# Kernel optimization log

Measured on AMD Instinct MI355X. Metric: run time of the kernel, lower is better.

The kernel has to match this reference:

```python
import jax, jax.numpy as jnp
import numpy as np

D_MODEL = 1024
N_HEADS = 16
D_K = D_MODEL // N_HEADS
B, S = 2, 2048
NEG = -1.0e9


def setup_inputs() -> dict:
    key = jax.random.key(0)
    ks = jax.random.split(key, 12)
    sc = 1.0 / np.sqrt(D_MODEL)
    inp = {
        'query': jax.random.normal(ks[0], (B, S, D_MODEL), jnp.float32),
        'key': jax.random.normal(ks[1], (B, S, D_MODEL), jnp.float32),
        'value': jax.random.normal(ks[2], (B, S, D_MODEL), jnp.float32),
        # causal mask, broadcast over batch: 1 = attend, 0 = masked
        'mask': jnp.broadcast_to(jnp.tril(jnp.ones((S, S), jnp.int32)), (B, S, S)),
        'wq': jax.random.normal(ks[3], (D_MODEL, D_MODEL), jnp.float32) * sc,
        'bq': jnp.zeros((D_MODEL,), jnp.float32),
        'wk': jax.random.normal(ks[4], (D_MODEL, D_MODEL), jnp.float32) * sc,
        'bk': jnp.zeros((D_MODEL,), jnp.float32),
        'wv': jax.random.normal(ks[5], (D_MODEL, D_MODEL), jnp.float32) * sc,
        'bv': jnp.zeros((D_MODEL,), jnp.float32),
        'wo': jax.random.normal(ks[6], (D_MODEL, D_MODEL), jnp.float32) * sc,
        'bo': jnp.zeros((D_MODEL,), jnp.float32),
    }
    return inp


def reference(query, key, value, mask, wq, bq, wk, bk, wv, bv, wo, bo):
    b, sq, _ = query.shape
    sk = key.shape[1]
    # linear projections, split into heads: [B, H, S, d_k]
    def proj(x, w, bias, s):
        return (x @ w + bias).reshape(b, s, N_HEADS, D_K).transpose(0, 2, 1, 3)
    Q = proj(query, wq, bq, sq)
    K = proj(key, wk, bk, sk)
    V = proj(value, wv, bv, sk)
    # scaled dot-product attention with full score matrix [B, H, Sq, Sk]
    scores = jnp.einsum('bhqd,bhkd->bhqk', Q, K) / np.sqrt(D_K)
    scores = jnp.where(mask[:, None, :, :] == 0, NEG, scores)
    attn = jax.nn.softmax(scores, axis=-1)
    ctx = jnp.einsum('bhqk,bhkd->bhqd', attn, V)
    ctx = ctx.transpose(0, 2, 1, 3).reshape(b, sq, D_MODEL)
    return ctx @ wo + bo
```

## Files before the change

### kernel.cpp

```cpp
#include <hip/hip_runtime.h>
#include <stdint.h>

#define AS1 __attribute__((address_space(1)))
#define AS3 __attribute__((address_space(3)))

typedef __attribute__((ext_vector_type(8))) __bf16 bf16x8;
typedef __attribute__((ext_vector_type(4))) float f32x4;
typedef __attribute__((ext_vector_type(4))) unsigned int u32x4;
typedef __attribute__((ext_vector_type(2))) unsigned int u32x2;

static __device__ __forceinline__ void gload16(const void* g, void* l) {
    __builtin_amdgcn_global_load_lds((AS1 void*)(uintptr_t)g, (AS3 void*)l, 16, 0, 0);
}

static __device__ __forceinline__ unsigned cvt_pk_bf16(float lo, float hi) {
    unsigned r;
    asm volatile("v_cvt_pk_bf16_f32 %0, %1, %2" : "=v"(r) : "v"(lo), "v"(hi));
    return r;
}
static __device__ __forceinline__ unsigned short f2bf(float f) {
    return (unsigned short)(cvt_pk_bf16(f, 0.f) & 0xffffu);
}

static __device__ __forceinline__ f32x4 mfma16(bf16x8 a, bf16x8 b, f32x4 c) {
    return __builtin_amdgcn_mfma_f32_16x16x32_bf16(a, b, c, 0, 0, 0);
}

static __device__ __forceinline__ float fexp2(float x) {
    return __builtin_amdgcn_exp2f(x);
}

__global__ __launch_bounds__(256) void k_wtrans4(const float* __restrict__ w0,
                                                 const float* __restrict__ w1,
                                                 const float* __restrict__ w2,
                                                 const float* __restrict__ w3,
                                                 unsigned short* __restrict__ o0,
                                                 unsigned short* __restrict__ o1,
                                                 unsigned short* __restrict__ o2,
                                                 unsigned short* __restrict__ o3) {
    const float* W;
    unsigned short* Wt;
    switch (blockIdx.z) {
        case 0: W = w0; Wt = o0; break;
        case 1: W = w1; Wt = o1; break;
        case 2: W = w2; Wt = o2; break;
        default: W = w3; Wt = o3; break;
    }
    __shared__ unsigned short tile[64][72];
    const int tid = threadIdx.x;
    const int k0 = blockIdx.x * 64, n0 = blockIdx.y * 64;
#pragma unroll
    for (int j = 0; j < 4; ++j) {
        int c = j * 256 + tid;
        int kr = c >> 4, c4 = c & 15;
        f32x4 v = *(const f32x4*)(W + (size_t)(k0 + kr) * 1024 + n0 + c4 * 4);
#pragma unroll
        for (int e = 0; e < 4; ++e) tile[c4 * 4 + e][kr] = f2bf(v[e]);
    }
    __syncthreads();
#pragma unroll
    for (int j = 0; j < 2; ++j) {
        int c = j * 256 + tid;
        int nr = c >> 3, kc = c & 7;
        union { unsigned short s[8]; u32x4 v; } t;
#pragma unroll
        for (int e = 0; e < 8; ++e) t.s[e] = tile[nr][kc * 8 + e];
        *(u32x4*)(Wt + (size_t)(n0 + nr) * 1024 + k0 + kc * 8) = t.v;
    }
}

__global__ __launch_bounds__(256) void k_cvt3(const float* __restrict__ q,
                                              const float* __restrict__ k,
                                              const float* __restrict__ v,
                                              unsigned short* __restrict__ oq,
                                              unsigned short* __restrict__ ok,
                                              unsigned short* __restrict__ ov) {
    const float* src; unsigned short* dst;
    switch (blockIdx.z) {
        case 0: src = q; dst = oq; break;
        case 1: src = k; dst = ok; break;
        default: src = v; dst = ov; break;
    }
    const size_t i = ((size_t)blockIdx.x * 256 + threadIdx.x) * 8;
    f32x4 a = *(const f32x4*)(src + i);
    f32x4 b = *(const f32x4*)(src + i + 4);
    u32x4 o;
    o[0] = cvt_pk_bf16(a[0], a[1]);
    o[1] = cvt_pk_bf16(a[2], a[3]);
    o[2] = cvt_pk_bf16(b[0], b[1]);
    o[3] = cvt_pk_bf16(b[2], b[3]);
    *(u32x4*)(dst + i) = o;
}

template <int A_F32, int OUT_F32>
static __device__ __forceinline__ void gemm_body(const void* __restrict__ Ap,
                                                 const unsigned short* __restrict__ Bt,
                                                 const float* __restrict__ bias,
                                                 void* __restrict__ Cp,
                                                 int M, int N, int K, float cscale,
                                                 char* smem) {
    constexpr int ASZ = A_F32 ? 16384 : 8192;
    char* sA = smem;
    char* sB = smem + 2 * ASZ;
    const int tid = threadIdx.x;
    const int wave = tid >> 6, lane = tid & 63, g = lane >> 4, l16 = lane & 15;
    const int wm = wave & 1, wn = wave >> 1;
    const int m0 = blockIdx.x * 64, n0 = blockIdx.y * 128;

    f32x4 acc[2][4];
#pragma unroll
    for (int i = 0; i < 2; ++i)
#pragma unroll
        for (int j = 0; j < 4; ++j) acc[i][j] = (f32x4){0.f, 0.f, 0.f, 0.f};

    auto STAGE = [&](int k0, int buf) {
        if constexpr (A_F32) {
            const float* A = (const float*)Ap;
            char* dst = sA + buf * ASZ;
#pragma unroll
            for (int j = 0; j < 4; ++j) {
                int c = j * 256 + tid;
                int row = c >> 4, w = c & 15, kc = w ^ (row & 15);
                gload16(A + (size_t)(m0 + row) * K + k0 + kc * 4, dst + c * 16);
            }
        } else {
            const unsigned short* A = (const unsigned short*)Ap;
            char* dst = sA + buf * ASZ;
#pragma unroll
            for (int j = 0; j < 2; ++j) {
                int c = j * 256 + tid;
                int row = c >> 3, w = c & 7, kc = w ^ (row & 7);
                gload16(A + (size_t)(m0 + row) * K + k0 + kc * 8, dst + c * 16);
            }
        }
        char* dst = sB + buf * 16384;
#pragma unroll
        for (int j = 0; j < 4; ++j) {
            int c = j * 256 + tid;
            int row = c >> 3, w = c & 7, kc = w ^ (row & 7);
            gload16(Bt + (size_t)(n0 + row) * K + k0 + kc * 8, dst + c * 16);
        }
    };

    const int nkt = K >> 6;
    STAGE(0, 0);
    __syncthreads();
    int cur = 0;
#pragma unroll 1
    for (int kt = 0; kt < nkt; ++kt) {
        if (kt + 1 < nkt) STAGE((kt + 1) << 6, cur ^ 1);
        const char* sAc = sA + cur * ASZ;
        const char* sBc = sB + cur * 16384;
#pragma unroll
        for (int ks = 0; ks < 2; ++ks) {
            bf16x8 af[2];
#pragma unroll
            for (int mi = 0; mi < 2; ++mi) {
                int row = wm * 32 + mi * 16 + l16;
                if constexpr (A_F32) {
                    int c0 = (ks * 8 + g * 2) ^ (row & 15);
                    int c1 = (ks * 8 + g * 2 + 1) ^ (row & 15);
                    f32x4 lo = *(const f32x4*)(sAc + row * 256 + c0 * 16);
                    f32x4 hi = *(const f32x4*)(sAc + row * 256 + c1 * 16);
                    union { unsigned u[4]; bf16x8 v; } cv;
                    cv.u[0] = cvt_pk_bf16(lo[0], lo[1]);
                    cv.u[1] = cvt_pk_bf16(lo[2], lo[3]);
                    cv.u[2] = cvt_pk_bf16(hi[0], hi[1]);
                    cv.u[3] = cvt_pk_bf16(hi[2], hi[3]);
                    af[mi] = cv.v;
                } else {
                    int c = (ks * 4 + g) ^ (row & 7);
                    af[mi] = *(const bf16x8*)(sAc + row * 128 + c * 16);
                }
            }
#pragma unroll
            for (int ni = 0; ni < 4; ++ni) {
                int row = wn * 64 + ni * 16 + l16;
                int c = (ks * 4 + g) ^ (row & 7);
                bf16x8 bfr = *(const bf16x8*)(sBc + row * 128 + c * 16);
#pragma unroll
                for (int mi = 0; mi < 2; ++mi)
                    acc[mi][ni] = mfma16(af[mi], bfr, acc[mi][ni]);
            }
        }
        __syncthreads();
        cur ^= 1;
    }
#pragma unroll
    for (int ni = 0; ni < 4; ++ni) {
        int col = n0 + wn * 64 + ni * 16 + l16;
        float bn = bias[col];
#pragma unroll
        for (int mi = 0; mi < 2; ++mi) {
            int rbase = m0 + wm * 32 + mi * 16 + g * 4;
#pragma unroll
            for (int r = 0; r < 4; ++r) {
                float v = (acc[mi][ni][r] + bn) * cscale;
                if constexpr (OUT_F32)
                    ((float*)Cp)[(size_t)(rbase + r) * N + col] = v;
                else
                    ((unsigned short*)Cp)[(size_t)(rbase + r) * N + col] = f2bf(v);
            }
        }
    }
}

__global__ __launch_bounds__(256) void k_gemm_qkv(
    const unsigned short* __restrict__ Aq, const unsigned short* __restrict__ Ak,
    const unsigned short* __restrict__ Av,
    const unsigned short* __restrict__ Wq, const unsigned short* __restrict__ Wk,
    const unsigned short* __restrict__ Wv,
    const float* __restrict__ bq, const float* __restrict__ bk, const float* __restrict__ bv,
    unsigned short* __restrict__ Q2, unsigned short* __restrict__ K2,
    unsigned short* __restrict__ V2) {
    extern __shared__ __align__(16) char smem[];
    const unsigned short* A; const unsigned short* Bt; const float* bias;
    unsigned short* C; float sc;
    switch (blockIdx.z) {
        case 0:  A = Aq; Bt = Wq; bias = bq; C = Q2; sc = 0.18033688011112042f; break;
        case 1:  A = Ak; Bt = Wk; bias = bk; C = K2; sc = 1.0f; break;
        default: A = Av; Bt = Wv; bias = bv; C = V2; sc = 1.0f; break;
    }
    gemm_body<0, 0>(A, Bt, bias, C, 4096, 1024, 1024, sc, smem);
}

__global__ __launch_bounds__(256) void k_gemm_o(const unsigned short* __restrict__ ctx,
                                                const unsigned short* __restrict__ Wo,
                                                const float* __restrict__ bo,
                                                float* __restrict__ out) {
    extern __shared__ __align__(16) char smem[];
    gemm_body<0, 1>(ctx, Wo, bo, out, 4096, 1024, 1024, 1.0f, smem);
}

__global__ __launch_bounds__(256) void k_vtrans(const unsigned short* __restrict__ V2,
                                                unsigned short* __restrict__ Vt) {
    __shared__ unsigned short tile[64][72];
    const int tid = threadIdx.x;
    const int s0 = blockIdx.x * 64;
    const int bh = blockIdx.y, b = bh >> 4, h = bh & 15;
#pragma unroll
    for (int j = 0; j < 2; ++j) {
        int c = j * 256 + tid;
        int sr = c >> 3, dc = c & 7;
        union { u32x4 v; unsigned short s[8]; } t;
        t.v = *(const u32x4*)(V2 + (size_t)(b * 2048 + s0 + sr) * 1024 + h * 64 + dc * 8);
#pragma unroll
        for (int e = 0; e < 8; ++e) tile[dc * 8 + e][sr] = t.s[e];
    }
    __syncthreads();
#pragma unroll
    for (int j = 0; j < 2; ++j) {
        int c = j * 256 + tid;
        int dr = c >> 3, sc = c & 7;
        union { unsigned short s[8]; u32x4 v; } t;
#pragma unroll
        for (int e = 0; e < 8; ++e) t.s[e] = tile[dr][sc * 8 + e];
        *(u32x4*)(Vt + ((size_t)bh * 64 + dr) * 2048 + s0 + sc * 8) = t.v;
    }
}

__global__ __launch_bounds__(128) void k_attn(const unsigned short* __restrict__ Q2,
                                              const unsigned short* __restrict__ K2,
                                              const unsigned short* __restrict__ Vt,
                                              unsigned short* __restrict__ ctx) {
    __shared__ __align__(16) char sK[8192];
    __shared__ __align__(16) char sV[2][8192];
    __shared__ __align__(16) char sP[2][2048];

    const int tid = threadIdx.x, w = tid >> 6, lane = tid & 63;
    const int g = lane >> 4, l16 = lane & 15;
    const int bid = blockIdx.x;
    const int xcd = bid & 7, j = bid >> 3;
    const int bh = xcd * 4 + (j & 3);
    const int p = j >> 2;
    const int b = bh >> 4, h = bh & 15;
    const int swzl = (l16 & 7) << 4;

    const int r0 = tid >> 3;
    const int sc0 = (tid & 7) ^ (r0 & 7);
    const unsigned short* ksrc = K2 + (size_t)(b * 2048 + r0) * 1024 + h * 64 + sc0 * 8;
    const unsigned short* vsrc = Vt + ((size_t)bh * 64 + r0) * 2048 + sc0 * 8;
    char* const myp = sP[w];
    char* const mypw = myp + l16 * 128;

#pragma unroll 1
    for (int t2 = 0; t2 < 2; ++t2) {
        const int t = t2 ? p : (63 - p);
        const int wq0 = t * 32 + w * 16;
        const int qg = wq0 + l16;

        const unsigned short* qp = Q2 + (size_t)(b * 2048 + wq0 + l16) * 1024 + h * 64;
        bf16x8 qf0 = *(const bf16x8*)(qp + g * 8);
        bf16x8 qf1 = *(const bf16x8*)(qp + 32 + g * 8);

        f32x4 accO[4];
#pragma unroll
        for (int i = 0; i < 4; ++i) accO[i] = (f32x4){0.f, 0.f, 0.f, 0.f};
        float m = 0.f, lsum = 0.f;

        const int nkv = (t >> 1) + 1;
        const int diag = t >> 1;
        __syncthreads();
#pragma unroll
        for (int rr = 0; rr < 4; ++rr) {
            gload16(ksrc + (size_t)(rr * 16) * 1024, sK + rr * 2048 + tid * 16);
            gload16(vsrc + (size_t)(rr * 16) * 2048, sV[0] + rr * 2048 + tid * 16);
        }
        __syncthreads();

        const unsigned short* kstage = ksrc + 64 * 1024;
        const unsigned short* vstage = vsrc + 64;

#pragma unroll 1
        for (int kt = 0; kt < nkv; ++kt) {
            const int cur = kt & 1;
            const int kv0 = kt * 64;
            float s[16];
            __builtin_amdgcn_s_setprio(1);
#pragma unroll
            for (int blk = 0; blk < 4; ++blk) {
                const int rl = blk * 16 + l16;
                const char* krow = sK + rl * 128;
                bf16x8 kf0 = *(const bf16x8*)(krow + ((g << 4) ^ swzl));
                bf16x8 kf1 = *(const bf16x8*)(krow + (((4 + g) << 4) ^ swzl));
                f32x4 a = (f32x4){0.f, 0.f, 0.f, 0.f};
                a = mfma16(kf0, qf0, a);
                a = mfma16(kf1, qf1, a);
#pragma unroll
                for (int rr = 0; rr < 4; ++rr) s[blk * 4 + rr] = a[rr];
            }
            __builtin_amdgcn_s_setprio(0);
            __syncthreads();
            if (kt + 1 < nkv) {
#pragma unroll
                for (int rr = 0; rr < 4; ++rr) {
                    gload16(kstage + (size_t)(rr * 16) * 1024, sK + rr * 2048 + tid * 16);
                    gload16(vstage + (size_t)(rr * 16) * 2048, sV[cur ^ 1] + rr * 2048 + tid * 16);
                }
                kstage += 64 * 1024;
                vstage += 64;
            }
            if (kt == diag) {
#pragma unroll
                for (int j2 = 0; j2 < 16; ++j2) {
                    int kvg = kv0 + (j2 >> 2) * 16 + g * 4 + (j2 & 3);
                    if (kvg > qg) s[j2] = -1e9f;
                }
            }
            float ps0 = 0.f, ps1 = 0.f, ps2 = 0.f, ps3 = 0.f;
            unsigned pk[8];
#pragma unroll
            for (int j2 = 0; j2 < 4; ++j2) {
                float a0 = fexp2(s[4 * j2] - m);
                float a1 = fexp2(s[4 * j2 + 1] - m);
                float a2 = fexp2(s[4 * j2 + 2] - m);
                float a3 = fexp2(s[4 * j2 + 3] - m);
                ps0 += a0; ps1 += a1; ps2 += a2; ps3 += a3;
                pk[2 * j2] = cvt_pk_bf16(a0, a1);
                pk[2 * j2 + 1] = cvt_pk_bf16(a2, a3);
            }
            float ps = (ps0 + ps1) + (ps2 + ps3);
            if (__any(ps > 16777216.f)) {
                float c1 = fmaxf(fmaxf(s[0], s[1]), s[2]);
                c1 = fmaxf(fmaxf(c1, s[3]), s[4]);
                c1 = fmaxf(fmaxf(c1, s[5]), s[6]);
                c1 = fmaxf(c1, s[7]);
                float c2 = fmaxf(fmaxf(s[8], s[9]), s[10]);
                c2 = fmaxf(fmaxf(c2, s[11]), s[12]);
                c2 = fmaxf(fmaxf(c2, s[13]), s[14]);
                c2 = fmaxf(c2, s[15]);
                float mx = fmaxf(c1, c2);
                mx = fmaxf(mx, __shfl_xor(mx, 16));
                mx = fmaxf(mx, __shfl_xor(mx, 32));
                float mnew = fmaxf(m, mx);
                float scl = fexp2(m - mnew);
                lsum *= scl;
#pragma unroll
                for (int dt = 0; dt < 4; ++dt) accO[dt] = accO[dt] * scl;
                m = mnew;
                ps = 0.f;
#pragma unroll
                for (int j2 = 0; j2 < 8; ++j2) {
                    float p0 = fexp2(s[2 * j2] - m);
                    float p1 = fexp2(s[2 * j2 + 1] - m);
                    ps += p0 + p1;
                    pk[j2] = cvt_pk_bf16(p0, p1);
                }
            }
            lsum += ps;
#pragma unroll
            for (int blk = 0; blk < 4; ++blk) {
                u32x2 pw = {pk[blk * 2], pk[blk * 2 + 1]};
                *(u32x2*)(mypw + ((blk * 32 + g * 8) ^ swzl)) = pw;
            }
            __builtin_amdgcn_s_setprio(1);
#pragma unroll
            for (int kvh = 0; kvh < 2; ++kvh) {
                bf16x8 pf = *(const bf16x8*)(mypw + ((kvh * 64 + g * 16) ^ swzl));
#pragma unroll
                for (int dt = 0; dt < 4; ++dt) {
                    const int rv = dt * 16 + l16;
                    bf16x8 vf = *(const bf16x8*)(sV[cur] + rv * 128 + (((kvh * 4 + g) << 4) ^ swzl));
                    accO[dt] = mfma16(vf, pf, accO[dt]);
                }
            }
            __builtin_amdgcn_s_setprio(0);
            __syncthreads();
        }
        float v = lsum;
        v += __shfl_xor(v, 16);
        v += __shfl_xor(v, 32);
        float inv = 1.f / v;
        unsigned short* cp = ctx + (size_t)(b * 2048 + wq0 + l16) * 1024 + h * 64 + g * 4;
#pragma unroll
        for (int dt = 0; dt < 4; ++dt) {
            u32x2 o;
            o[0] = cvt_pk_bf16(accO[dt][0] * inv, accO[dt][1] * inv);
            o[1] = cvt_pk_bf16(accO[dt][2] * inv, accO[dt][3] * inv);
            *(u32x2*)(cp + dt * 16) = o;
        }
    }
}

extern "C" void kernel_launch(void* const* d_in, const int* in_sizes, int n_in,
                              void* d_out, int out_size, void* d_ws, size_t ws_size,
                              hipStream_t stream) {
    const float* query = (const float*)d_in[0];
    const float* key   = (const float*)d_in[1];
    const float* value = (const float*)d_in[2];
    const float* wq = (const float*)d_in[4];
    const float* bq = (const float*)d_in[5];
    const float* wk = (const float*)d_in[6];
    const float* bk = (const float*)d_in[7];
    const float* wv = (const float*)d_in[8];
    const float* bv = (const float*)d_in[9];
    const float* wo = (const float*)d_in[10];
    const float* bo = (const float*)d_in[11];
    float* out = (float*)d_out;

    char* ws = (char*)d_ws;
    unsigned short* Wtq = (unsigned short*)ws;
    unsigned short* Wtk = Wtq + 1024 * 1024;
    unsigned short* Wtv = Wtk + 1024 * 1024;
    unsigned short* Wto = Wtv + 1024 * 1024;
    unsigned short* Q2  = Wto + 1024 * 1024;
    unsigned short* K2  = Q2 + 4096 * 1024;
    unsigned short* V2  = K2 + 4096 * 1024;
    unsigned short* Aq  = V2 + 4096 * 1024;
    unsigned short* Ak  = Aq + 4096 * 1024;
    unsigned short* Av  = Ak + 4096 * 1024;
    unsigned short* Vt  = Aq;
    unsigned short* ctx = Ak;

    dim3 blk(256);
    k_wtrans4<<<dim3(16, 16, 4), blk, 0, stream>>>(wq, wk, wv, wo, Wtq, Wtk, Wtv, Wto);
    k_cvt3<<<dim3(2048, 1, 3), blk, 0, stream>>>(query, key, value, Aq, Ak, Av);

    k_gemm_qkv<<<dim3(64, 8, 3), blk, 49152, stream>>>(Aq, Ak, Av,
                                                       Wtq, Wtk, Wtv, bq, bk, bv,
                                                       Q2, K2, V2);

    k_vtrans<<<dim3(32, 32), blk, 0, stream>>>(V2, Vt);
    k_attn<<<dim3(1024), dim3(128), 0, stream>>>(Q2, K2, Vt, ctx);

    k_gemm_o<<<dim3(64, 8), blk, 49152, stream>>>(ctx, Wto, bo, out);
}
```

Measured before the change: 116.0 us.

## Process 64-row query tile per block with two row groups per wave

The attention kernel no longer walks two balanced 32-row query tiles per block one after the other. Each block now handles a single 64-row query tile, and each wave computes two 16-row groups against every K/V tile staged in shared memory. This halves the K/V global-to-LDS traffic and the barrier count per query row, and doubles the MFMA work per LDS read of K and V. In exchange, blocks now carry uneven causal work (mitigated by launching the heaviest tiles first) and each thread holds more registers, which can lower occupancy.

```diff
diff --git a/kernel.cpp b/kernel.cpp
--- a/kernel.cpp
+++ b/kernel.cpp
@@ -265,14 +265,14 @@
                                               unsigned short* __restrict__ ctx) {
     __shared__ __align__(16) char sK[8192];
     __shared__ __align__(16) char sV[2][8192];
-    __shared__ __align__(16) char sP[2][2048];
+    __shared__ __align__(16) char sP[2][2][2048];
 
     const int tid = threadIdx.x, w = tid >> 6, lane = tid & 63;
     const int g = lane >> 4, l16 = lane & 15;
     const int bid = blockIdx.x;
     const int xcd = bid & 7, j = bid >> 3;
     const int bh = xcd * 4 + (j & 3);
-    const int p = j >> 2;
+    const int t = 31 - (j >> 2);
     const int b = bh >> 4, h = bh & 15;
     const int swzl = (l16 & 7) << 4;
 
@@ -280,145 +280,195 @@
     const int sc0 = (tid & 7) ^ (r0 & 7);
     const unsigned short* ksrc = K2 + (size_t)(b * 2048 + r0) * 1024 + h * 64 + sc0 * 8;
     const unsigned short* vsrc = Vt + ((size_t)bh * 64 + r0) * 2048 + sc0 * 8;
-    char* const myp = sP[w];
-    char* const mypw = myp + l16 * 128;
+    char* const myp0 = sP[w][0] + l16 * 128;
+    char* const myp1 = sP[w][1] + l16 * 128;
+
+    const int wq0 = t * 64 + w * 32;
+    const int qg0 = wq0 + l16, qg1 = wq0 + 16 + l16;
+
+    const unsigned short* qp0 = Q2 + (size_t)(b * 2048 + wq0 + l16) * 1024 + h * 64;
+    const unsigned short* qp1 = qp0 + 16 * 1024;
+    bf16x8 qf00 = *(const bf16x8*)(qp0 + g * 8);
+    bf16x8 qf01 = *(const bf16x8*)(qp0 + 32 + g * 8);
+    bf16x8 qf10 = *(const bf16x8*)(qp1 + g * 8);
+    bf16x8 qf11 = *(const bf16x8*)(qp1 + 32 + g * 8);
+
+    f32x4 accO0[4], accO1[4];
+#pragma unroll
+    for (int i = 0; i < 4; ++i) {
+        accO0[i] = (f32x4){0.f, 0.f, 0.f, 0.f};
+        accO1[i] = (f32x4){0.f, 0.f, 0.f, 0.f};
+    }
+    float m0 = 0.f, m1 = 0.f, lsum0 = 0.f, lsum1 = 0.f;
+
+    const int nkv = t + 1;
+#pragma unroll
+    for (int rr = 0; rr < 4; ++rr) {
+        gload16(ksrc + (size_t)(rr * 16) * 1024, sK + rr * 2048 + tid * 16);
+        gload16(vsrc + (size_t)(rr * 16) * 2048, sV[0] + rr * 2048 + tid * 16);
+    }
+    __syncthreads();
+
+    const unsigned short* kstage = ksrc + 64 * 1024;
+    const unsigned short* vstage = vsrc + 64;
 
 #pragma unroll 1
-    for (int t2 = 0; t2 < 2; ++t2) {
-        const int t = t2 ? p : (63 - p);
-        const int wq0 = t * 32 + w * 16;
-        const int qg = wq0 + l16;
-
-        const unsigned short* qp = Q2 + (size_t)(b * 2048 + wq0 + l16) * 1024 + h * 64;
-        bf16x8 qf0 = *(const bf16x8*)(qp + g * 8);
-        bf16x8 qf1 = *(const bf16x8*)(qp + 32 + g * 8);
-
-        f32x4 accO[4];
-#pragma unroll
-        for (int i = 0; i < 4; ++i) accO[i] = (f32x4){0.f, 0.f, 0.f, 0.f};
-        float m = 0.f, lsum = 0.f;
-
-        const int nkv = (t >> 1) + 1;
-        const int diag = t >> 1;
+    for (int kt = 0; kt < nkv; ++kt) {
+        const int cur = kt & 1;
+        const int kv0 = kt * 64;
+        float s0[16], s1[16];
+        __builtin_amdgcn_s_setprio(1);
+#pragma unroll
+        for (int blk = 0; blk < 4; ++blk) {
+            const int rl = blk * 16 + l16;
+            const char* krow = sK + rl * 128;
+            bf16x8 kf0 = *(const bf16x8*)(krow + ((g << 4) ^ swzl));
+            bf16x8 kf1 = *(const bf16x8*)(krow + (((4 + g) << 4) ^ swzl));
+            f32x4 a0 = (f32x4){0.f, 0.f, 0.f, 0.f};
+            a0 = mfma16(kf0, qf00, a0);
+            a0 = mfma16(kf1, qf01, a0);
+            f32x4 a1 = (f32x4){0.f, 0.f, 0.f, 0.f};
+            a1 = mfma16(kf0, qf10, a1);
+            a1 = mfma16(kf1, qf11, a1);
+#pragma unroll
+            for (int rr = 0; rr < 4; ++rr) {
+                s0[blk * 4 + rr] = a0[rr];
+                s1[blk * 4 + rr] = a1[rr];
+            }
+        }
+        __builtin_amdgcn_s_setprio(0);
         __syncthreads();
-#pragma unroll
-        for (int rr = 0; rr < 4; ++rr) {
-            gload16(ksrc + (size_t)(rr * 16) * 1024, sK + rr * 2048 + tid * 16);
-            gload16(vsrc + (size_t)(rr * 16) * 2048, sV[0] + rr * 2048 + tid * 16);
-        }
-        __syncthreads();
-
-        const unsigned short* kstage = ksrc + 64 * 1024;
-        const unsigned short* vstage = vsrc + 64;
-
-#pragma unroll 1
-        for (int kt = 0; kt < nkv; ++kt) {
-            const int cur = kt & 1;
-            const int kv0 = kt * 64;
-            float s[16];
-            __builtin_amdgcn_s_setprio(1);
-#pragma unroll
-            for (int blk = 0; blk < 4; ++blk) {
-                const int rl = blk * 16 + l16;
-                const char* krow = sK + rl * 128;
-                bf16x8 kf0 = *(const bf16x8*)(krow + ((g << 4) ^ swzl));
-                bf16x8 kf1 = *(const bf16x8*)(krow + (((4 + g) << 4) ^ swzl));
-                f32x4 a = (f32x4){0.f, 0.f, 0.f, 0.f};
-                a = mfma16(kf0, qf0, a);
-                a = mfma16(kf1, qf1, a);
-#pragma unroll
-                for (int rr = 0; rr < 4; ++rr) s[blk * 4 + rr] = a[rr];
-            }
-            __builtin_amdgcn_s_setprio(0);
-            __syncthreads();
-            if (kt + 1 < nkv) {
-#pragma unroll
-                for (int rr = 0; rr < 4; ++rr) {
-                    gload16(kstage + (size_t)(rr * 16) * 1024, sK + rr * 2048 + tid * 16);
-                    gload16(vstage + (size_t)(rr * 16) * 2048, sV[cur ^ 1] + rr * 2048 + tid * 16);
-                }
-                kstage += 64 * 1024;
-                vstage += 64;
-            }
-            if (kt == diag) {
-#pragma unroll
-                for (int j2 = 0; j2 < 16; ++j2) {
-                    int kvg = kv0 + (j2 >> 2) * 16 + g * 4 + (j2 & 3);
-                    if (kvg > qg) s[j2] = -1e9f;
-                }
-            }
-            float ps0 = 0.f, ps1 = 0.f, ps2 = 0.f, ps3 = 0.f;
-            unsigned pk[8];
-#pragma unroll
-            for (int j2 = 0; j2 < 4; ++j2) {
-                float a0 = fexp2(s[4 * j2] - m);
-                float a1 = fexp2(s[4 * j2 + 1] - m);
-                float a2 = fexp2(s[4 * j2 + 2] - m);
-                float a3 = fexp2(s[4 * j2 + 3] - m);
-                ps0 += a0; ps1 += a1; ps2 += a2; ps3 += a3;
-                pk[2 * j2] = cvt_pk_bf16(a0, a1);
-                pk[2 * j2 + 1] = cvt_pk_bf16(a2, a3);
-            }
-            float ps = (ps0 + ps1) + (ps2 + ps3);
-            if (__any(ps > 16777216.f)) {
-                float c1 = fmaxf(fmaxf(s[0], s[1]), s[2]);
-                c1 = fmaxf(fmaxf(c1, s[3]), s[4]);
-                c1 = fmaxf(fmaxf(c1, s[5]), s[6]);
-                c1 = fmaxf(c1, s[7]);
-                float c2 = fmaxf(fmaxf(s[8], s[9]), s[10]);
-                c2 = fmaxf(fmaxf(c2, s[11]), s[12]);
-                c2 = fmaxf(fmaxf(c2, s[13]), s[14]);
-                c2 = fmaxf(c2, s[15]);
+        if (kt + 1 < nkv) {
+#pragma unroll
+            for (int rr = 0; rr < 4; ++rr) {
+                gload16(kstage + (size_t)(rr * 16) * 1024, sK + rr * 2048 + tid * 16);
+                gload16(vstage + (size_t)(rr * 16) * 2048, sV[cur ^ 1] + rr * 2048 + tid * 16);
+            }
+            kstage += 64 * 1024;
+            vstage += 64;
+        }
+        if (kt == t) {
+#pragma unroll
+            for (int j2 = 0; j2 < 16; ++j2) {
+                int kvg = kv0 + (j2 >> 2) * 16 + g * 4 + (j2 & 3);
+                if (kvg > qg0) s0[j2] = -1e9f;
+                if (kvg > qg1) s1[j2] = -1e9f;
+            }
+        }
+        float pa0 = 0.f, pa1 = 0.f, pa2 = 0.f, pa3 = 0.f;
+        float pb0 = 0.f, pb1 = 0.f, pb2 = 0.f, pb3 = 0.f;
+        unsigned pk0[8], pk1[8];
+#pragma unroll
+        for (int j2 = 0; j2 < 4; ++j2) {
+            float a0 = fexp2(s0[4 * j2] - m0);
+            float a1 = fexp2(s0[4 * j2 + 1] - m0);
+            float a2 = fexp2(s0[4 * j2 + 2] - m0);
+            float a3 = fexp2(s0[4 * j2 + 3] - m0);
+            pa0 += a0; pa1 += a1; pa2 += a2; pa3 += a3;
+            pk0[2 * j2] = cvt_pk_bf16(a0, a1);
+            pk0[2 * j2 + 1] = cvt_pk_bf16(a2, a3);
+            float b0 = fexp2(s1[4 * j2] - m1);
+            float b1 = fexp2(s1[4 * j2 + 1] - m1);
+            float b2 = fexp2(s1[4 * j2 + 2] - m1);
+            float b3 = fexp2(s1[4 * j2 + 3] - m1);
+            pb0 += b0; pb1 += b1; pb2 += b2; pb3 += b3;
+            pk1[2 * j2] = cvt_pk_bf16(b0, b1);
+            pk1[2 * j2 + 1] = cvt_pk_bf16(b2, b3);
+        }
+        float ps0 = (pa0 + pa1) + (pa2 + pa3);
+        float ps1 = (pb0 + pb1) + (pb2 + pb3);
+        if (__any(fmaxf(ps0, ps1) > 16777216.f)) {
+            {
+                float c1 = fmaxf(fmaxf(s0[0], s0[1]), fmaxf(s0[2], s0[3]));
+                c1 = fmaxf(c1, fmaxf(fmaxf(s0[4], s0[5]), fmaxf(s0[6], s0[7])));
+                float c2 = fmaxf(fmaxf(s0[8], s0[9]), fmaxf(s0[10], s0[11]));
+                c2 = fmaxf(c2, fmaxf(fmaxf(s0[12], s0[13]), fmaxf(s0[14], s0[15])));
                 float mx = fmaxf(c1, c2);
                 mx = fmaxf(mx, __shfl_xor(mx, 16));
                 mx = fmaxf(mx, __shfl_xor(mx, 32));
-                float mnew = fmaxf(m, mx);
-                float scl = fexp2(m - mnew);
-                lsum *= scl;
-#pragma unroll
-                for (int dt = 0; dt < 4; ++dt) accO[dt] = accO[dt] * scl;
-                m = mnew;
-                ps = 0.f;
+                float mnew = fmaxf(m0, mx);
+                float scl = fexp2(m0 - mnew);
+                lsum0 *= scl;
+#pragma unroll
+                for (int dt = 0; dt < 4; ++dt) accO0[dt] = accO0[dt] * scl;
+                m0 = mnew;
+                ps0 = 0.f;
 #pragma unroll
                 for (int j2 = 0; j2 < 8; ++j2) {
-                    float p0 = fexp2(s[2 * j2] - m);
-                    float p1 = fexp2(s[2 * j2 + 1] - m);
-                    ps += p0 + p1;
-                    pk[j2] = cvt_pk_bf16(p0, p1);
+                    float p0 = fexp2(s0[2 * j2] - m0);
+                    float p1 = fexp2(s0[2 * j2 + 1] - m0);
+                    ps0 += p0 + p1;
+                    pk0[j2] = cvt_pk_bf16(p0, p1);
                 }
             }
-            lsum += ps;
-#pragma unroll
-            for (int blk = 0; blk < 4; ++blk) {
-                u32x2 pw = {pk[blk * 2], pk[blk * 2 + 1]};
-                *(u32x2*)(mypw + ((blk * 32 + g * 8) ^ swzl)) = pw;
-            }
-            __builtin_amdgcn_s_setprio(1);
-#pragma unroll
-            for (int kvh = 0; kvh < 2; ++kvh) {
-                bf16x8 pf = *(const bf16x8*)(mypw + ((kvh * 64 + g * 16) ^ swzl));
-#pragma unroll
-                for (int dt = 0; dt < 4; ++dt) {
-                    const int rv = dt * 16 + l16;
-                    bf16x8 vf = *(const bf16x8*)(sV[cur] + rv * 128 + (((kvh * 4 + g) << 4) ^ swzl));
-                    accO[dt] = mfma16(vf, pf, accO[dt]);
+            {
+                float c1 = fmaxf(fmaxf(s1[0], s1[1]), fmaxf(s1[2], s1[3]));
+                c1 = fmaxf(c1, fmaxf(fmaxf(s1[4], s1[5]), fmaxf(s1[6], s1[7])));
+                float c2 = fmaxf(fmaxf(s1[8], s1[9]), fmaxf(s1[10], s1[11]));
+                c2 = fmaxf(c2, fmaxf(fmaxf(s1[12], s1[13]), fmaxf(s1[14], s1[15])));
+                float mx = fmaxf(c1, c2);
+                mx = fmaxf(mx, __shfl_xor(mx, 16));
+                mx = fmaxf(mx, __shfl_xor(mx, 32));
+                float mnew = fmaxf(m1, mx);
+                float scl = fexp2(m1 - mnew);
+                lsum1 *= scl;
+#pragma unroll
+                for (int dt = 0; dt < 4; ++dt) accO1[dt] = accO1[dt] * scl;
+                m1 = mnew;
+                ps1 = 0.f;
+#pragma unroll
+                for (int j2 = 0; j2 < 8; ++j2) {
+                    float p0 = fexp2(s1[2 * j2] - m1);
+                    float p1 = fexp2(s1[2 * j2 + 1] - m1);
+                    ps1 += p0 + p1;
+                    pk1[j2] = cvt_pk_bf16(p0, p1);
                 }
             }
-            __builtin_amdgcn_s_setprio(0);
-            __syncthreads();
-        }
-        float v = lsum;
-        v += __shfl_xor(v, 16);
-        v += __shfl_xor(v, 32);
-        float inv = 1.f / v;
-        unsigned short* cp = ctx + (size_t)(b * 2048 + wq0 + l16) * 1024 + h * 64 + g * 4;
-#pragma unroll
-        for (int dt = 0; dt < 4; ++dt) {
-            u32x2 o;
-            o[0] = cvt_pk_bf16(accO[dt][0] * inv, accO[dt][1] * inv);
-            o[1] = cvt_pk_bf16(accO[dt][2] * inv, accO[dt][3] * inv);
-            *(u32x2*)(cp + dt * 16) = o;
-        }
+        }
+        lsum0 += ps0;
+        lsum1 += ps1;
+#pragma unroll
+        for (int blk = 0; blk < 4; ++blk) {
+            u32x2 pw0 = {pk0[blk * 2], pk0[blk * 2 + 1]};
+            u32x2 pw1 = {pk1[blk * 2], pk1[blk * 2 + 1]};
+            *(u32x2*)(myp0 + ((blk * 32 + g * 8) ^ swzl)) = pw0;
+            *(u32x2*)(myp1 + ((blk * 32 + g * 8) ^ swzl)) = pw1;
+        }
+        __builtin_amdgcn_s_setprio(1);
+#pragma unroll
+        for (int kvh = 0; kvh < 2; ++kvh) {
+            bf16x8 pf0 = *(const bf16x8*)(myp0 + ((kvh * 64 + g * 16) ^ swzl));
+            bf16x8 pf1 = *(const bf16x8*)(myp1 + ((kvh * 64 + g * 16) ^ swzl));
+#pragma unroll
+            for (int dt = 0; dt < 4; ++dt) {
+                const int rv = dt * 16 + l16;
+                bf16x8 vf = *(const bf16x8*)(sV[cur] + rv * 128 + (((kvh * 4 + g) << 4) ^ swzl));
+                accO0[dt] = mfma16(vf, pf0, accO0[dt]);
+                accO1[dt] = mfma16(vf, pf1, accO1[dt]);
+            }
+        }
+        __builtin_amdgcn_s_setprio(0);
+        __syncthreads();
+    }
+    float v0 = lsum0;
+    v0 += __shfl_xor(v0, 16);
+    v0 += __shfl_xor(v0, 32);
+    float inv0 = 1.f / v0;
+    float v1 = lsum1;
+    v1 += __shfl_xor(v1, 16);
+    v1 += __shfl_xor(v1, 32);
+    float inv1 = 1.f / v1;
+    unsigned short* cp0 = ctx + (size_t)(b * 2048 + wq0 + l16) * 1024 + h * 64 + g * 4;
+    unsigned short* cp1 = cp0 + 16 * 1024;
+#pragma unroll
+    for (int dt = 0; dt < 4; ++dt) {
+        u32x2 o0, o1;
+        o0[0] = cvt_pk_bf16(accO0[dt][0] * inv0, accO0[dt][1] * inv0);
+        o0[1] = cvt_pk_bf16(accO0[dt][2] * inv0, accO0[dt][3] * inv0);
+        o1[0] = cvt_pk_bf16(accO1[dt][0] * inv1, accO1[dt][1] * inv1);
+        o1[1] = cvt_pk_bf16(accO1[dt][2] * inv1, accO1[dt][3] * inv1);
+        *(u32x2*)(cp0 + dt * 16) = o0;
+        *(u32x2*)(cp1 + dt * 16) = o1;
     }
 }
 
```

Result: no change. 116.1 us (+0.1%).

## Merge prep kernels and switch GEMMs to 128x128 single-buffered tiles

Applied to the files above, without the earlier changes.

Combines the weight transpose and activation bf16 conversion into one launch, removing a kernel launch. Enlarges the GEMM block tile from 64x128 to 128x128 so each wave computes 4x4 MFMA tiles, which improves operand reuse from LDS. The tile loads lose their double buffering and now synchronize before and after each load, which exposes global-load latency. The larger tiles also halve the number of blocks, lowering occupancy on a GPU with many CUs.

```diff
diff --git a/kernel.cpp b/kernel.cpp
--- a/kernel.cpp
+++ b/kernel.cpp
@@ -30,169 +30,125 @@
     return __builtin_amdgcn_exp2f(x);
 }
 
-__global__ __launch_bounds__(256) void k_wtrans4(const float* __restrict__ w0,
-                                                 const float* __restrict__ w1,
-                                                 const float* __restrict__ w2,
-                                                 const float* __restrict__ w3,
-                                                 unsigned short* __restrict__ o0,
-                                                 unsigned short* __restrict__ o1,
-                                                 unsigned short* __restrict__ o2,
-                                                 unsigned short* __restrict__ o3) {
-    const float* W;
-    unsigned short* Wt;
-    switch (blockIdx.z) {
-        case 0: W = w0; Wt = o0; break;
-        case 1: W = w1; Wt = o1; break;
-        case 2: W = w2; Wt = o2; break;
-        default: W = w3; Wt = o3; break;
-    }
+__global__ __launch_bounds__(256) void k_prep(
+    const float* __restrict__ w0, const float* __restrict__ w1,
+    const float* __restrict__ w2, const float* __restrict__ w3,
+    const float* __restrict__ aq, const float* __restrict__ ak,
+    const float* __restrict__ av,
+    unsigned short* __restrict__ o0, unsigned short* __restrict__ o1,
+    unsigned short* __restrict__ o2, unsigned short* __restrict__ o3,
+    unsigned short* __restrict__ cq, unsigned short* __restrict__ ck,
+    unsigned short* __restrict__ cv) {
     __shared__ unsigned short tile[64][72];
     const int tid = threadIdx.x;
-    const int k0 = blockIdx.x * 64, n0 = blockIdx.y * 64;
-#pragma unroll
-    for (int j = 0; j < 4; ++j) {
-        int c = j * 256 + tid;
-        int kr = c >> 4, c4 = c & 15;
-        f32x4 v = *(const f32x4*)(W + (size_t)(k0 + kr) * 1024 + n0 + c4 * 4);
-#pragma unroll
-        for (int e = 0; e < 4; ++e) tile[c4 * 4 + e][kr] = f2bf(v[e]);
-    }
-    __syncthreads();
-#pragma unroll
-    for (int j = 0; j < 2; ++j) {
-        int c = j * 256 + tid;
-        int nr = c >> 3, kc = c & 7;
-        union { unsigned short s[8]; u32x4 v; } t;
-#pragma unroll
-        for (int e = 0; e < 8; ++e) t.s[e] = tile[nr][kc * 8 + e];
-        *(u32x4*)(Wt + (size_t)(n0 + nr) * 1024 + k0 + kc * 8) = t.v;
-    }
-}
-
-__global__ __launch_bounds__(256) void k_cvt3(const float* __restrict__ q,
-                                              const float* __restrict__ k,
-                                              const float* __restrict__ v,
-                                              unsigned short* __restrict__ oq,
-                                              unsigned short* __restrict__ ok,
-                                              unsigned short* __restrict__ ov) {
-    const float* src; unsigned short* dst;
-    switch (blockIdx.z) {
-        case 0: src = q; dst = oq; break;
-        case 1: src = k; dst = ok; break;
-        default: src = v; dst = ov; break;
-    }
-    const size_t i = ((size_t)blockIdx.x * 256 + threadIdx.x) * 8;
-    f32x4 a = *(const f32x4*)(src + i);
-    f32x4 b = *(const f32x4*)(src + i + 4);
-    u32x4 o;
-    o[0] = cvt_pk_bf16(a[0], a[1]);
-    o[1] = cvt_pk_bf16(a[2], a[3]);
-    o[2] = cvt_pk_bf16(b[0], b[1]);
-    o[3] = cvt_pk_bf16(b[2], b[3]);
-    *(u32x4*)(dst + i) = o;
-}
-
-template <int A_F32, int OUT_F32>
-static __device__ __forceinline__ void gemm_body(const void* __restrict__ Ap,
-                                                 const unsigned short* __restrict__ Bt,
-                                                 const float* __restrict__ bias,
-                                                 void* __restrict__ Cp,
-                                                 int M, int N, int K, float cscale,
-                                                 char* smem) {
-    constexpr int ASZ = A_F32 ? 16384 : 8192;
-    char* sA = smem;
-    char* sB = smem + 2 * ASZ;
+    const int bid = blockIdx.x;
+    if (bid < 1024) {
+        const float* W;
+        unsigned short* Wt;
+        switch (bid >> 8) {
+            case 0: W = w0; Wt = o0; break;
+            case 1: W = w1; Wt = o1; break;
+            case 2: W = w2; Wt = o2; break;
+            default: W = w3; Wt = o3; break;
+        }
+        const int xy = bid & 255;
+        const int k0 = (xy & 15) * 64, n0 = (xy >> 4) * 64;
+#pragma unroll
+        for (int j = 0; j < 4; ++j) {
+            int c = j * 256 + tid;
+            int kr = c >> 4, c4 = c & 15;
+            f32x4 v = *(const f32x4*)(W + (size_t)(k0 + kr) * 1024 + n0 + c4 * 4);
+#pragma unroll
+            for (int e = 0; e < 4; ++e) tile[c4 * 4 + e][kr] = f2bf(v[e]);
+        }
+        __syncthreads();
+#pragma unroll
+        for (int j = 0; j < 2; ++j) {
+            int c = j * 256 + tid;
+            int nr = c >> 3, kc = c & 7;
+            union { unsigned short s[8]; u32x4 v; } t;
+#pragma unroll
+            for (int e = 0; e < 8; ++e) t.s[e] = tile[nr][kc * 8 + e];
+            *(u32x4*)(Wt + (size_t)(n0 + nr) * 1024 + k0 + kc * 8) = t.v;
+        }
+    } else {
+        const int c = bid - 1024;
+        const float* src; unsigned short* dst;
+        switch (c >> 11) {
+            case 0: src = aq; dst = cq; break;
+            case 1: src = ak; dst = ck; break;
+            default: src = av; dst = cv; break;
+        }
+        const size_t i = ((size_t)(c & 2047) * 256 + tid) * 8;
+        f32x4 a = *(const f32x4*)(src + i);
+        f32x4 b = *(const f32x4*)(src + i + 4);
+        u32x4 o;
+        o[0] = cvt_pk_bf16(a[0], a[1]);
+        o[1] = cvt_pk_bf16(a[2], a[3]);
+        o[2] = cvt_pk_bf16(b[0], b[1]);
+        o[3] = cvt_pk_bf16(b[2], b[3]);
+        *(u32x4*)(dst + i) = o;
+    }
+}
+
+template <int OUT_F32>
+static __device__ __forceinline__ void gemm128_body(
+    const unsigned short* __restrict__ A, const unsigned short* __restrict__ Bt,
+    const float* __restrict__ bias, void* __restrict__ Cp, float cscale,
+    char* sA, char* sB) {
     const int tid = threadIdx.x;
     const int wave = tid >> 6, lane = tid & 63, g = lane >> 4, l16 = lane & 15;
     const int wm = wave & 1, wn = wave >> 1;
-    const int m0 = blockIdx.x * 64, n0 = blockIdx.y * 128;
-
-    f32x4 acc[2][4];
-#pragma unroll
-    for (int i = 0; i < 2; ++i)
+    const int m0 = blockIdx.x * 128, n0 = blockIdx.y * 128;
+    const int K = 1024, N = 1024;
+
+    f32x4 acc[4][4];
+#pragma unroll
+    for (int i = 0; i < 4; ++i)
 #pragma unroll
         for (int j = 0; j < 4; ++j) acc[i][j] = (f32x4){0.f, 0.f, 0.f, 0.f};
 
-    auto STAGE = [&](int k0, int buf) {
-        if constexpr (A_F32) {
-            const float* A = (const float*)Ap;
-            char* dst = sA + buf * ASZ;
-#pragma unroll
-            for (int j = 0; j < 4; ++j) {
-                int c = j * 256 + tid;
-                int row = c >> 4, w = c & 15, kc = w ^ (row & 15);
-                gload16(A + (size_t)(m0 + row) * K + k0 + kc * 4, dst + c * 16);
-            }
-        } else {
-            const unsigned short* A = (const unsigned short*)Ap;
-            char* dst = sA + buf * ASZ;
-#pragma unroll
-            for (int j = 0; j < 2; ++j) {
-                int c = j * 256 + tid;
-                int row = c >> 3, w = c & 7, kc = w ^ (row & 7);
-                gload16(A + (size_t)(m0 + row) * K + k0 + kc * 8, dst + c * 16);
-            }
-        }
-        char* dst = sB + buf * 16384;
+#pragma unroll 1
+    for (int kt = 0; kt < 16; ++kt) {
+        const int k0 = kt << 6;
+        __syncthreads();
 #pragma unroll
         for (int j = 0; j < 4; ++j) {
             int c = j * 256 + tid;
-            int row = c >> 3, w = c & 7, kc = w ^ (row & 7);
-            gload16(Bt + (size_t)(n0 + row) * K + k0 + kc * 8, dst + c * 16);
-        }
-    };
-
-    const int nkt = K >> 6;
-    STAGE(0, 0);
-    __syncthreads();
-    int cur = 0;
-#pragma unroll 1
-    for (int kt = 0; kt < nkt; ++kt) {
-        if (kt + 1 < nkt) STAGE((kt + 1) << 6, cur ^ 1);
-        const char* sAc = sA + cur * ASZ;
-        const char* sBc = sB + cur * 16384;
+            int row = c >> 3, ch = c & 7, kc = ch ^ (row & 7);
+            gload16(A + (size_t)(m0 + row) * K + k0 + kc * 8, sA + c * 16);
+            gload16(Bt + (size_t)(n0 + row) * K + k0 + kc * 8, sB + c * 16);
+        }
+        __syncthreads();
 #pragma unroll
         for (int ks = 0; ks < 2; ++ks) {
-            bf16x8 af[2];
-#pragma unroll
-            for (int mi = 0; mi < 2; ++mi) {
-                int row = wm * 32 + mi * 16 + l16;
-                if constexpr (A_F32) {
-                    int c0 = (ks * 8 + g * 2) ^ (row & 15);
-                    int c1 = (ks * 8 + g * 2 + 1) ^ (row & 15);
-                    f32x4 lo = *(const f32x4*)(sAc + row * 256 + c0 * 16);
-                    f32x4 hi = *(const f32x4*)(sAc + row * 256 + c1 * 16);
-                    union { unsigned u[4]; bf16x8 v; } cv;
-                    cv.u[0] = cvt_pk_bf16(lo[0], lo[1]);
-                    cv.u[1] = cvt_pk_bf16(lo[2], lo[3]);
-                    cv.u[2] = cvt_pk_bf16(hi[0], hi[1]);
-                    cv.u[3] = cvt_pk_bf16(hi[2], hi[3]);
-                    af[mi] = cv.v;
-                } else {
-                    int c = (ks * 4 + g) ^ (row & 7);
-                    af[mi] = *(const bf16x8*)(sAc + row * 128 + c * 16);
-                }
+            bf16x8 af[4], bfr[4];
+#pragma unroll
+            for (int mi = 0; mi < 4; ++mi) {
+                int row = wm * 64 + mi * 16 + l16;
+                int c = (ks * 4 + g) ^ (row & 7);
+                af[mi] = *(const bf16x8*)(sA + row * 128 + c * 16);
             }
 #pragma unroll
             for (int ni = 0; ni < 4; ++ni) {
                 int row = wn * 64 + ni * 16 + l16;
                 int c = (ks * 4 + g) ^ (row & 7);
-                bf16x8 bfr = *(const bf16x8*)(sBc + row * 128 + c * 16);
-#pragma unroll
-                for (int mi = 0; mi < 2; ++mi)
-                    acc[mi][ni] = mfma16(af[mi], bfr, acc[mi][ni]);
-            }
-        }
-        __syncthreads();
-        cur ^= 1;
+                bfr[ni] = *(const bf16x8*)(sB + row * 128 + c * 16);
+            }
+#pragma unroll
+            for (int mi = 0; mi < 4; ++mi)
+#pragma unroll
+                for (int ni = 0; ni < 4; ++ni)
+                    acc[mi][ni] = mfma16(af[mi], bfr[ni], acc[mi][ni]);
+        }
     }
 #pragma unroll
     for (int ni = 0; ni < 4; ++ni) {
         int col = n0 + wn * 64 + ni * 16 + l16;
         float bn = bias[col];
 #pragma unroll
-        for (int mi = 0; mi < 2; ++mi) {
-            int rbase = m0 + wm * 32 + mi * 16 + g * 4;
+        for (int mi = 0; mi < 4; ++mi) {
+            int rbase = m0 + wm * 64 + mi * 16 + g * 4;
 #pragma unroll
             for (int r = 0; r < 4; ++r) {
                 float v = (acc[mi][ni][r] + bn) * cscale;
@@ -213,7 +169,7 @@
     const float* __restrict__ bq, const float* __restrict__ bk, const float* __restrict__ bv,
     unsigned short* __restrict__ Q2, unsigned short* __restrict__ K2,
     unsigned short* __restrict__ V2) {
-    extern __shared__ __align__(16) char smem[];
+    __shared__ __align__(16) char sA[16384], sB[16384];
     const unsigned short* A; const unsigned short* Bt; const float* bias;
     unsigned short* C; float sc;
     switch (blockIdx.z) {
@@ -221,15 +177,15 @@
         case 1:  A = Ak; Bt = Wk; bias = bk; C = K2; sc = 1.0f; break;
         default: A = Av; Bt = Wv; bias = bv; C = V2; sc = 1.0f; break;
     }
-    gemm_body<0, 0>(A, Bt, bias, C, 4096, 1024, 1024, sc, smem);
+    gemm128_body<0>(A, Bt, bias, C, sc, sA, sB);
 }
 
 __global__ __launch_bounds__(256) void k_gemm_o(const unsigned short* __restrict__ ctx,
                                                 const unsigned short* __restrict__ Wo,
                                                 const float* __restrict__ bo,
                                                 float* __restrict__ out) {
-    extern __shared__ __align__(16) char smem[];
-    gemm_body<0, 1>(ctx, Wo, bo, out, 4096, 1024, 1024, 1.0f, smem);
+    __shared__ __align__(16) char sA[16384], sB[16384];
+    gemm128_body<1>(ctx, Wo, bo, out, 1.0f, sA, sB);
 }
 
 __global__ __launch_bounds__(256) void k_vtrans(const unsigned short* __restrict__ V2,
@@ -453,15 +409,15 @@
     unsigned short* ctx = Ak;
 
     dim3 blk(256);
-    k_wtrans4<<<dim3(16, 16, 4), blk, 0, stream>>>(wq, wk, wv, wo, Wtq, Wtk, Wtv, Wto);
-    k_cvt3<<<dim3(2048, 1, 3), blk, 0, stream>>>(query, key, value, Aq, Ak, Av);
-
-    k_gemm_qkv<<<dim3(64, 8, 3), blk, 49152, stream>>>(Aq, Ak, Av,
-                                                       Wtq, Wtk, Wtv, bq, bk, bv,
-                                                       Q2, K2, V2);
+    k_prep<<<dim3(7168), blk, 0, stream>>>(wq, wk, wv, wo, query, key, value,
+                                           Wtq, Wtk, Wtv, Wto, Aq, Ak, Av);
+
+    k_gemm_qkv<<<dim3(32, 8, 3), blk, 0, stream>>>(Aq, Ak, Av,
+                                                   Wtq, Wtk, Wtv, bq, bk, bv,
+                                                   Q2, K2, V2);
 
     k_vtrans<<<dim3(32, 32), blk, 0, stream>>>(V2, Vt);
     k_attn<<<dim3(1024), dim3(128), 0, stream>>>(Q2, K2, Vt, ctx);
 
-    k_gemm_o<<<dim3(64, 8), blk, 49152, stream>>>(ctx, Wto, bo, out);
-}
+    k_gemm_o<<<dim3(32, 8), blk, 0, stream>>>(ctx, Wto, bo, out);
+}
```

Measured after the change: 128.5 us. 1.11x slower.
